# Performance work log

Measured on AMD Instinct MI355X. Metric: run time of the kernel, lower is better.

Reference implementation:

```python
import jax, jax.numpy as jnp
import numpy as np

N = 50000
D_IN = 128
D_OUT = 128
EPS = 1e-5


def setup_inputs() -> dict:
    key = jax.random.key(0)
    ks = jax.random.split(key, 10)
    x = jax.random.normal(ks[0], (N, D_IN), dtype=jnp.float32)
    edge_index = jax.random.randint(ks[1], (2, 800000), 0, N, dtype=jnp.int64)
    s_in = 1.0 / np.sqrt(D_IN)
    s_out = 1.0 / np.sqrt(D_OUT)
    return {
        "x": x,
        "edge_index": edge_index,
        # SAGEConv 1: lin_l (on aggregated neighbors, with bias), lin_r (root, no bias)
        "w1_l": jax.random.uniform(ks[2], (D_OUT, D_IN), jnp.float32, -s_in, s_in),
        "b1_l": jnp.zeros((D_OUT,), jnp.float32),
        "w1_r": jax.random.uniform(ks[3], (D_OUT, D_IN), jnp.float32, -s_in, s_in),
        # SAGEConv 2
        "w2_l": jax.random.uniform(ks[4], (D_OUT, D_OUT), jnp.float32, -s_out, s_out),
        "b2_l": jnp.zeros((D_OUT,), jnp.float32),
        "w2_r": jax.random.uniform(ks[5], (D_OUT, D_OUT), jnp.float32, -s_out, s_out),
        # BatchNorm affine params
        "bn_gamma": jnp.ones((D_OUT,), jnp.float32),
        "bn_beta": jnp.zeros((D_OUT,), jnp.float32),
    }


def _sage_conv(x, src, dst, w_l, b_l, w_r):
    # mean aggregation of source-node features into target nodes
    msg = x[src]                                              # [E, D]
    agg = jax.ops.segment_sum(msg, dst, num_segments=N)       # [N, D]
    cnt = jax.ops.segment_sum(jnp.ones((src.shape[0],), x.dtype), dst, num_segments=N)
    mean = agg / jnp.maximum(cnt, 1.0)[:, None]
    return mean @ w_l.T + b_l + x @ w_r.T


def _batch_norm(x, gamma, beta):
    mu = jnp.mean(x, axis=0)
    var = jnp.mean(jnp.square(x - mu), axis=0)  # biased, as in torch BN training
    return (x - mu) * jax.lax.rsqrt(var + EPS) * gamma + beta


def reference(x, edge_index, w1_l, b1_l, w1_r, w2_l, b2_l, w2_r, bn_gamma, bn_beta):
    src, dst = edge_index[0], edge_index[1]
    h = _sage_conv(x, src, dst, w1_l, b1_l, w1_r)
    h = _batch_norm(h, bn_gamma, bn_beta)
    h = jax.nn.relu(h)
    out = _sage_conv(h, src, dst, w2_l, b2_l, w2_r)
    return out
```

## Files before the change

kernel.cpp:

```cpp
#include <hip/hip_runtime.h>

#define D 128
#define EPS 1e-5f
#define FB_EPB 8

typedef unsigned int uint;
typedef __attribute__((ext_vector_type(4))) float f32x4;
typedef __attribute__((ext_vector_type(8))) short s16x8;

__device__ __forceinline__ uint pack_bf16(float a, float b)
{
    uint ua = __float_as_uint(a);
    uint ub = __float_as_uint(b);
    ua += 0x7FFFu + ((ua >> 16) & 1u);
    ub += 0x7FFFu + ((ub >> 16) & 1u);
    return (ua >> 16) | (ub & 0xFFFF0000u);
}
__device__ __forceinline__ float bf_lo(uint v) { return __uint_as_float(v << 16); }
__device__ __forceinline__ float bf_hi(uint v) { return __uint_as_float(v & 0xFFFF0000u); }

__global__ void prep_kernel(const float* __restrict__ x, uint* __restrict__ xb, int ncvt,
                            const float* __restrict__ w1l, const float* __restrict__ w1r,
                            const float* __restrict__ w2l, const float* __restrict__ w2r,
                            uint* __restrict__ wb1, uint* __restrict__ wb2)
{
    int idx = blockIdx.x * 256 + threadIdx.x;
    if (idx < ncvt) {
        float4 v = ((const float4*)x)[idx];
        uint2 o;
        o.x = pack_bf16(v.x, v.y);
        o.y = pack_bf16(v.z, v.w);
        ((uint2*)xb)[idx] = o;
    } else if (idx < ncvt + 8192) {
        int r = idx - ncvt;
        int layer = r >> 12;
        int rem = r & 4095;
        int lane = rem & 63;
        int knt = rem >> 6;
        int kstep = knt >> 3, nt = knt & 7;
        int nn = nt * 16 + (lane & 15);
        int kbase = kstep * 32 + (lane >> 4) * 8;
        const float* wl = layer ? w2l : w1l;
        const float* wr = layer ? w2r : w1r;
        uint* wb = layer ? wb2 : wb1;
        float v[8];
#pragma unroll
        for (int j = 0; j < 8; j++) {
            int k = kbase + j;
            v[j] = (k < D) ? wl[nn * D + k] : wr[nn * D + (k - D)];
        }
        uint4 o;
        o.x = pack_bf16(v[0], v[1]);
        o.y = pack_bf16(v[2], v[3]);
        o.z = pack_bf16(v[4], v[5]);
        o.w = pack_bf16(v[6], v[7]);
        ((uint4*)wb)[(kstep * 8 + nt) * 64 + lane] = o;
    }
}

__global__ __launch_bounds__(512) void bcount_kernel(const int* __restrict__ dst,
                                                     int* __restrict__ bcnt,
                                                     int E, int nblk, int nbuck)
{
    __shared__ int cnt[128];
    int t = threadIdx.x;
    if (t < 128) cnt[t] = 0;
    __syncthreads();
    int e0 = blockIdx.x * (512 * FB_EPB);
#pragma unroll
    for (int k = 0; k < FB_EPB; k++) {
        int e = e0 + k * 512 + t;
        if (e < E) atomicAdd(&cnt[dst[e] >> 9], 1);
    }
    __syncthreads();
    if (t < nbuck) bcnt[t * nblk + blockIdx.x] = cnt[t];
}

__global__ __launch_bounds__(1024) void bscan_kernel(int* __restrict__ bcnt, int M)
{
    __shared__ int sums[1024];
    int t = threadIdx.x;
    int chunk = (M + 1023) / 1024;
    int b0 = t * chunk;
    int b1 = min(b0 + chunk, M);
    int v[32];
    int s = 0;
    for (int i = b0; i < b1; i++) { v[i - b0] = bcnt[i]; s += v[i - b0]; }
    sums[t] = s;
    __syncthreads();
    for (int off = 1; off < 1024; off <<= 1) {
        int u = (t >= off) ? sums[t - off] : 0;
        __syncthreads();
        sums[t] += u;
        __syncthreads();
    }
    int run = sums[t] - s;
    for (int i = b0; i < b1; i++) { bcnt[i] = run; run += v[i - b0]; }
    if (t == 1023) bcnt[M] = sums[1023];
}

__global__ __launch_bounds__(512) void bscatter_kernel(const int* __restrict__ src,
                                                       const int* __restrict__ dst,
                                                       const int* __restrict__ bcnt,
                                                       uint2* __restrict__ ebuf,
                                                       int E, int nblk, int nbuck)
{
    __shared__ int cnt[128], base[128];
    int t = threadIdx.x;
    if (t < 128) cnt[t] = 0;
    __syncthreads();
    int e0 = blockIdx.x * (512 * FB_EPB);
    int s[FB_EPB], d[FB_EPB], loc[FB_EPB];
#pragma unroll
    for (int k = 0; k < FB_EPB; k++) {
        int e = e0 + k * 512 + t;
        if (e < E) {
            s[k] = src[e];
            d[k] = dst[e];
            loc[k] = atomicAdd(&cnt[d[k] >> 9], 1);
        }
    }
    __syncthreads();
    if (t < nbuck) base[t] = bcnt[t * nblk + blockIdx.x];
    __syncthreads();
#pragma unroll
    for (int k = 0; k < FB_EPB; k++) {
        int e = e0 + k * 512 + t;
        if (e < E) {
            int b = d[k] >> 9;
            ebuf[base[b] + loc[k]] = make_uint2((uint)s[k], (uint)d[k]);
        }
    }
}

__global__ __launch_bounds__(512) void pbuild_kernel(const int* __restrict__ bcnt,
                                                     const uint2* __restrict__ ebuf,
                                                     int* __restrict__ rowptr,
                                                     int* __restrict__ col,
                                                     int n, int nblk, int nbuck, int M, int E)
{
    __shared__ int lcnt[512], lscan[512];
    int t = threadIdx.x;
    int b = blockIdx.x;
    int nb = b << 9;
    int e0 = bcnt[b * nblk];
    int e1 = (b + 1 < nbuck) ? bcnt[(b + 1) * nblk] : bcnt[M];
    lcnt[t] = 0;
    __syncthreads();
    for (int i = e0 + t; i < e1; i += 512)
        atomicAdd(&lcnt[(int)ebuf[i].y - nb], 1);
    __syncthreads();
    int s = lcnt[t];
    lscan[t] = s;
    __syncthreads();
    for (int off = 1; off < 512; off <<= 1) {
        int u = (t >= off) ? lscan[t - off] : 0;
        __syncthreads();
        lscan[t] += u;
        __syncthreads();
    }
    int start = e0 + lscan[t] - s;
    int ncnt = min(512, n - nb);
    if (t < ncnt) rowptr[nb + t] = start;
    if (b == nbuck - 1 && t == 0) rowptr[n] = E;
    lscan[t] = start;
    __syncthreads();
    for (int i = e0 + t; i < e1; i += 512) {
        uint2 ed = ebuf[i];
        int p = atomicAdd(&lscan[(int)ed.y - nb], 1);
        col[p] = (int)ed.x;
    }
}

template<bool BN>
__global__ __launch_bounds__(256) void agg_kernel(const int* __restrict__ rowptr,
                                                  const int* __restrict__ col,
                                                  const uint* __restrict__ featb,
                                                  const float* __restrict__ scsh,
                                                  uint* __restrict__ aggb, int n)
{
    int node = blockIdx.x * 4 + (threadIdx.x >> 6);
    if (node >= n) return;
    int lane = threadIdx.x & 63;
    int sub = lane >> 4, l16 = lane & 15;
    int r0 = rowptr[node], r1 = rowptr[node + 1];
    uint4* out4 = (uint4*)aggb;
    if (r0 == r1) {
        if (lane < 16) out4[(size_t)node * 16 + l16] = make_uint4(0, 0, 0, 0);
        return;
    }
    float sc[8], sh[8];
    if (BN) {
        float4 s0 = ((const float4*)scsh)[l16 * 2];
        float4 s1 = ((const float4*)scsh)[l16 * 2 + 1];
        float4 t0 = ((const float4*)scsh)[32 + l16 * 2];
        float4 t1 = ((const float4*)scsh)[32 + l16 * 2 + 1];
        sc[0] = s0.x; sc[1] = s0.y; sc[2] = s0.z; sc[3] = s0.w;
        sc[4] = s1.x; sc[5] = s1.y; sc[6] = s1.z; sc[7] = s1.w;
        sh[0] = t0.x; sh[1] = t0.y; sh[2] = t0.z; sh[3] = t0.w;
        sh[4] = t1.x; sh[5] = t1.y; sh[6] = t1.z; sh[7] = t1.w;
    }
    float acc[8] = {0.f, 0.f, 0.f, 0.f, 0.f, 0.f, 0.f, 0.f};
    const uint4* fb = (const uint4*)featb;
    int last = r1 - 1;

    for (int i = r0; i < r1; i += 32) {
        uint4 v[8];
#pragma unroll
        for (int r = 0; r < 8; r++) {
            int idx = i + r * 4 + sub;
            int c = col[min(idx, last)];
            v[r] = fb[(size_t)c * 16 + l16];
        }
#pragma unroll
        for (int r = 0; r < 8; r++) {
            bool valid = (i + r * 4 + sub) < r1;
            uint4 u = v[r];
            float e[8] = {bf_lo(u.x), bf_hi(u.x), bf_lo(u.y), bf_hi(u.y),
                          bf_lo(u.z), bf_hi(u.z), bf_lo(u.w), bf_hi(u.w)};
#pragma unroll
            for (int j = 0; j < 8; j++) {
                float t = e[j];
                if (BN) t = fmaxf(t * sc[j] + sh[j], 0.f);
                acc[j] += valid ? t : 0.f;
            }
        }
    }
#pragma unroll
    for (int j = 0; j < 8; j++) {
        acc[j] += __shfl_down(acc[j], 32);
        acc[j] += __shfl_down(acc[j], 16);
    }
    if (lane < 16) {
        float inv = 1.0f / (float)(r1 - r0);
        uint4 o;
        o.x = pack_bf16(acc[0] * inv, acc[1] * inv);
        o.y = pack_bf16(acc[2] * inv, acc[3] * inv);
        o.z = pack_bf16(acc[4] * inv, acc[5] * inv);
        o.w = pack_bf16(acc[6] * inv, acc[7] * inv);
        out4[(size_t)node * 16 + l16] = o;
    }
}

#define TSTRIDE 132
template<bool FUSE1, bool BNP2>
__global__ __launch_bounds__(256) void conv_kernel(
    const uint* __restrict__ p1b, const uint* __restrict__ p2b,
    const uint* __restrict__ wb, const float* __restrict__ bias,
    const float* __restrict__ scsh, float* __restrict__ outf,
    uint* __restrict__ outb, float* __restrict__ pstats, int n)
{
    extern __shared__ float smem[];
    float* tile = smem;
    float* scs = smem;
    int w = threadIdx.x >> 6, lane = threadIdx.x & 63;
    int quad = lane >> 4, l15 = lane & 15;
    int nb = blockIdx.x * 64;

    if (BNP2) {
        scs[threadIdx.x] = scsh[threadIdx.x];
        __syncthreads();
    }

    const uint4* p1 = (const uint4*)p1b;
    const uint4* p2 = (const uint4*)p2b;
    const uint4* wv = (const uint4*)wb;

    uint4 B[8][2];
    int nt0 = w * 2;
#pragma unroll
    for (int ks = 0; ks < 8; ks++) {
#pragma unroll
        for (int t = 0; t < 2; t++)
            B[ks][t] = wv[(ks * 8 + nt0 + t) * 64 + lane];
    }

    float bv0 = bias[nt0 * 16 + l15];
    float bv1 = bias[nt0 * 16 + 16 + l15];

    for (int rt = 0; rt < 4; rt++) {
        int node = nb + rt * 16 + l15;
        int nc = min(node, n - 1);
        uint4 A[8];
#pragma unroll
        for (int ks = 0; ks < 4; ks++) A[ks] = p1[(size_t)nc * 16 + ks * 4 + quad];
#pragma unroll
        for (int ks = 0; ks < 4; ks++) A[ks + 4] = p2[(size_t)nc * 16 + ks * 4 + quad];

        if (BNP2) {
#pragma unroll
            for (int ks = 4; ks < 8; ks++) {
                int c0 = (ks - 4) * 32 + quad * 8;
                uint4 u = A[ks];
                float e[8] = {bf_lo(u.x), bf_hi(u.x), bf_lo(u.y), bf_hi(u.y),
                              bf_lo(u.z), bf_hi(u.z), bf_lo(u.w), bf_hi(u.w)};
#pragma unroll
                for (int j = 0; j < 8; j++)
                    e[j] = fmaxf(e[j] * scs[c0 + j] + scs[128 + c0 + j], 0.f);
                u.x = pack_bf16(e[0], e[1]);
                u.y = pack_bf16(e[2], e[3]);
                u.z = pack_bf16(e[4], e[5]);
                u.w = pack_bf16(e[6], e[7]);
                A[ks] = u;
            }
        }

        f32x4 acc0 = {bv0, bv0, bv0, bv0};
        f32x4 acc1 = {bv1, bv1, bv1, bv1};
#pragma unroll
        for (int ks = 0; ks < 8; ks++) {
            s16x8 a = *(s16x8*)&A[ks];
            acc0 = __builtin_amdgcn_mfma_f32_16x16x32_bf16(a, *(s16x8*)&B[ks][0], acc0, 0, 0, 0);
            acc1 = __builtin_amdgcn_mfma_f32_16x16x32_bf16(a, *(s16x8*)&B[ks][1], acc1, 0, 0, 0);
        }
        int row0 = nb + rt * 16 + quad * 4;
        int colbase = nt0 * 16 + l15;
        if (FUSE1) {
            int rloc0 = rt * 16 + quad * 4;
#pragma unroll
            for (int reg = 0; reg < 4; reg++) {
                bool ok = (row0 + reg) < n;
                tile[(rloc0 + reg) * TSTRIDE + colbase]      = ok ? acc0[reg] : 0.f;
                tile[(rloc0 + reg) * TSTRIDE + colbase + 16] = ok ? acc1[reg] : 0.f;
            }
        } else {
#pragma unroll
            for (int reg = 0; reg < 4; reg++) {
                int row = row0 + reg;
                if (row < n) {
                    outf[(size_t)row * D + colbase] = acc0[reg];
                    outf[(size_t)row * D + colbase + 16] = acc1[reg];
                }
            }
        }
    }

    if (FUSE1) {
        __syncthreads();
        int colj = threadIdx.x & 127, half = threadIdx.x >> 7;
        float s = 0.f, ss = 0.f;
        for (int r = half * 32; r < half * 32 + 32; r++) {
            float v = tile[r * TSTRIDE + colj];
            s += v;
            ss += v * v;
        }
        float* pb = pstats + (size_t)blockIdx.x * 512 + half * 256;
        pb[colj] = s;
        pb[128 + colj] = ss;
        uint4* ob4 = (uint4*)outb;
#pragma unroll
        for (int q4 = 0; q4 < 4; q4++) {
            int idx = q4 * 256 + threadIdx.x;
            int r = idx >> 4, q = idx & 15;
            int row = nb + r;
            if (row < n) {
                float* tr = &tile[r * TSTRIDE + q * 8];
                uint4 o;
                o.x = pack_bf16(tr[0], tr[1]);
                o.y = pack_bf16(tr[2], tr[3]);
                o.z = pack_bf16(tr[4], tr[5]);
                o.w = pack_bf16(tr[6], tr[7]);
                ob4[(size_t)row * 16 + q] = o;
            }
        }
    }
}

__global__ __launch_bounds__(256) void reduce_kernel(const float* __restrict__ pstats,
                                                     float* __restrict__ stats, int nparts)
{
    int j = threadIdx.x;
    int chunk = (nparts + gridDim.x - 1) / gridDim.x;
    int p0 = blockIdx.x * chunk;
    int p1 = min(p0 + chunk, nparts);
    float s = 0.f;
    for (int p = p0; p < p1; p++) s += pstats[(size_t)p * 256 + j];
    unsafeAtomicAdd(&stats[j], s);
}

__global__ void bnfin_kernel(const float* __restrict__ stats, const float* __restrict__ gamma,
                             const float* __restrict__ beta, float* __restrict__ scsh, float n_inv)
{
    int j = threadIdx.x;
    float mean = stats[j] * n_inv;
    float var = fmaxf(stats[128 + j] * n_inv - mean * mean, 0.f);
    float sc = gamma[j] * rsqrtf(var + EPS);
    scsh[j] = sc;
    scsh[128 + j] = beta[j] - mean * sc;
}

extern "C" void kernel_launch(void* const* d_in, const int* in_sizes, int n_in,
                              void* d_out, int out_size, void* d_ws, size_t ws_size,
                              hipStream_t stream)
{
    const float* x     = (const float*)d_in[0];
    const int*   ei    = (const int*)d_in[1];
    const float* w1_l  = (const float*)d_in[2];
    const float* b1_l  = (const float*)d_in[3];
    const float* w1_r  = (const float*)d_in[4];
    const float* w2_l  = (const float*)d_in[5];
    const float* b2_l  = (const float*)d_in[6];
    const float* w2_r  = (const float*)d_in[7];
    const float* gamma = (const float*)d_in[8];
    const float* beta  = (const float*)d_in[9];

    int N = in_sizes[0] / D;
    int E = in_sizes[1] / 2;
    const int* src = ei;
    const int* dst = ei + E;

    int cblocks = (N + 63) / 64;
    int nbuck   = (N + 511) >> 9;
    int nblk    = (E + 4095) / 4096;
    int M       = nbuck * nblk;

    uint*  aggb   = (uint*)d_ws;
    uint*  xb     = aggb + (size_t)N * 64;
    uint*  hb     = xb + (size_t)N * 64;
    uint*  wb1    = hb + (size_t)N * 64;
    uint*  wb2    = wb1 + 16384;
    uint2* ebuf   = (uint2*)(wb2 + 16384);
    float* stats  = (float*)(ebuf + E);
    float* scsh   = stats + 256;
    float* pstats = scsh + 256;
    int*   rowptr = (int*)(pstats + (size_t)cblocks * 512);
    int*   col    = rowptr + N + 1;
    int*   bcnt   = col + E;

    hipMemsetAsync(stats, 0, 256 * sizeof(float), stream);

    int ncvt = N * 32;
    int pblocks = (ncvt + 8192 + 255) / 256;
    prep_kernel<<<pblocks, 256, 0, stream>>>(x, xb, ncvt, w1_l, w1_r, w2_l, w2_r, wb1, wb2);

    int ablocks = (N + 3) / 4;

    bcount_kernel<<<nblk, 512, 0, stream>>>(dst, bcnt, E, nblk, nbuck);
    bscan_kernel<<<1, 1024, 0, stream>>>(bcnt, M);
    bscatter_kernel<<<nblk, 512, 0, stream>>>(src, dst, bcnt, ebuf, E, nblk, nbuck);
    pbuild_kernel<<<nbuck, 512, 0, stream>>>(bcnt, ebuf, rowptr, col, N, nblk, nbuck, M, E);

    agg_kernel<false><<<ablocks, 256, 0, stream>>>(rowptr, col, xb, nullptr, aggb, N);
    conv_kernel<true, false><<<cblocks, 256, 64 * TSTRIDE * 4, stream>>>(
        aggb, xb, wb1, b1_l, nullptr, nullptr, hb, pstats, N);

    reduce_kernel<<<32, 256, 0, stream>>>(pstats, stats, cblocks * 2);
    bnfin_kernel<<<1, 128, 0, stream>>>(stats, gamma, beta, scsh, 1.0f / (float)N);

    agg_kernel<true><<<ablocks, 256, 0, stream>>>(rowptr, col, hb, scsh, aggb, N);
    conv_kernel<false, true><<<cblocks, 256, 256 * 4, stream>>>(
        aggb, hb, wb2, b2_l, scsh, (float*)d_out, nullptr, nullptr, N);
}
```

Baseline: 265.2 us.

## Materialize BN+ReLU once in a separate pass and simplify gather loop with zero-row padding

Adds a bnapply kernel that writes normalized, ReLU'd bf16 features once, so the second aggregation and second conv no longer recompute BN+ReLU for every gathered edge. The gather loop drops from 8 to 4 rows per iteration. Invalid edges now point at an appended zero row instead of being masked with a select. The cost is an extra N×128 bf16 read/write pass, one more launch, and extra workspace for the padded buffers.

```diff
diff --git a/kernel.cpp b/kernel.cpp
--- a/kernel.cpp
+++ b/kernel.cpp
@@ -55,6 +55,8 @@
         o.z = pack_bf16(v[4], v[5]);
         o.w = pack_bf16(v[6], v[7]);
         ((uint4*)wb)[(kstep * 8 + nt) * 64 + lane] = o;
+    } else if (idx < ncvt + 8192 + 32) {
+        ((uint2*)xb)[ncvt + (idx - ncvt - 8192)] = make_uint2(0, 0);
     }
 }
 
@@ -172,11 +174,9 @@
     }
 }
 
-template<bool BN>
 __global__ __launch_bounds__(256) void agg_kernel(const int* __restrict__ rowptr,
                                                   const int* __restrict__ col,
                                                   const uint* __restrict__ featb,
-                                                  const float* __restrict__ scsh,
                                                   uint* __restrict__ aggb, int n)
 {
     int node = blockIdx.x * 4 + (threadIdx.x >> 6);
@@ -189,41 +189,26 @@
         if (lane < 16) out4[(size_t)node * 16 + l16] = make_uint4(0, 0, 0, 0);
         return;
     }
-    float sc[8], sh[8];
-    if (BN) {
-        float4 s0 = ((const float4*)scsh)[l16 * 2];
-        float4 s1 = ((const float4*)scsh)[l16 * 2 + 1];
-        float4 t0 = ((const float4*)scsh)[32 + l16 * 2];
-        float4 t1 = ((const float4*)scsh)[32 + l16 * 2 + 1];
-        sc[0] = s0.x; sc[1] = s0.y; sc[2] = s0.z; sc[3] = s0.w;
-        sc[4] = s1.x; sc[5] = s1.y; sc[6] = s1.z; sc[7] = s1.w;
-        sh[0] = t0.x; sh[1] = t0.y; sh[2] = t0.z; sh[3] = t0.w;
-        sh[4] = t1.x; sh[5] = t1.y; sh[6] = t1.z; sh[7] = t1.w;
-    }
     float acc[8] = {0.f, 0.f, 0.f, 0.f, 0.f, 0.f, 0.f, 0.f};
     const uint4* fb = (const uint4*)featb;
     int last = r1 - 1;
 
-    for (int i = r0; i < r1; i += 32) {
-        uint4 v[8];
-#pragma unroll
-        for (int r = 0; r < 8; r++) {
+    for (int i = r0; i < r1; i += 16) {
+        uint4 v[4];
+#pragma unroll
+        for (int r = 0; r < 4; r++) {
             int idx = i + r * 4 + sub;
-            int c = col[min(idx, last)];
+            int cl = col[min(idx, last)];
+            int c = (idx < r1) ? cl : n;
             v[r] = fb[(size_t)c * 16 + l16];
         }
 #pragma unroll
-        for (int r = 0; r < 8; r++) {
-            bool valid = (i + r * 4 + sub) < r1;
+        for (int r = 0; r < 4; r++) {
             uint4 u = v[r];
-            float e[8] = {bf_lo(u.x), bf_hi(u.x), bf_lo(u.y), bf_hi(u.y),
-                          bf_lo(u.z), bf_hi(u.z), bf_lo(u.w), bf_hi(u.w)};
-#pragma unroll
-            for (int j = 0; j < 8; j++) {
-                float t = e[j];
-                if (BN) t = fmaxf(t * sc[j] + sh[j], 0.f);
-                acc[j] += valid ? t : 0.f;
-            }
+            acc[0] += bf_lo(u.x); acc[1] += bf_hi(u.x);
+            acc[2] += bf_lo(u.y); acc[3] += bf_hi(u.y);
+            acc[4] += bf_lo(u.z); acc[5] += bf_hi(u.z);
+            acc[6] += bf_lo(u.w); acc[7] += bf_hi(u.w);
         }
     }
 #pragma unroll
@@ -243,24 +228,18 @@
 }
 
 #define TSTRIDE 132
-template<bool FUSE1, bool BNP2>
+template<bool FUSE1>
 __global__ __launch_bounds__(256) void conv_kernel(
     const uint* __restrict__ p1b, const uint* __restrict__ p2b,
     const uint* __restrict__ wb, const float* __restrict__ bias,
-    const float* __restrict__ scsh, float* __restrict__ outf,
-    uint* __restrict__ outb, float* __restrict__ pstats, int n)
+    float* __restrict__ outf, uint* __restrict__ outb,
+    float* __restrict__ pstats, int n)
 {
     extern __shared__ float smem[];
     float* tile = smem;
-    float* scs = smem;
     int w = threadIdx.x >> 6, lane = threadIdx.x & 63;
     int quad = lane >> 4, l15 = lane & 15;
     int nb = blockIdx.x * 64;
-
-    if (BNP2) {
-        scs[threadIdx.x] = scsh[threadIdx.x];
-        __syncthreads();
-    }
 
     const uint4* p1 = (const uint4*)p1b;
     const uint4* p2 = (const uint4*)p2b;
@@ -286,24 +265,6 @@
         for (int ks = 0; ks < 4; ks++) A[ks] = p1[(size_t)nc * 16 + ks * 4 + quad];
 #pragma unroll
         for (int ks = 0; ks < 4; ks++) A[ks + 4] = p2[(size_t)nc * 16 + ks * 4 + quad];
-
-        if (BNP2) {
-#pragma unroll
-            for (int ks = 4; ks < 8; ks++) {
-                int c0 = (ks - 4) * 32 + quad * 8;
-                uint4 u = A[ks];
-                float e[8] = {bf_lo(u.x), bf_hi(u.x), bf_lo(u.y), bf_hi(u.y),
-                              bf_lo(u.z), bf_hi(u.z), bf_lo(u.w), bf_hi(u.w)};
-#pragma unroll
-                for (int j = 0; j < 8; j++)
-                    e[j] = fmaxf(e[j] * scs[c0 + j] + scs[128 + c0 + j], 0.f);
-                u.x = pack_bf16(e[0], e[1]);
-                u.y = pack_bf16(e[2], e[3]);
-                u.z = pack_bf16(e[4], e[5]);
-                u.w = pack_bf16(e[6], e[7]);
-                A[ks] = u;
-            }
-        }
 
         f32x4 acc0 = {bv0, bv0, bv0, bv0};
         f32x4 acc1 = {bv1, bv1, bv1, bv1};
@@ -389,6 +350,29 @@
     scsh[128 + j] = beta[j] - mean * sc;
 }
 
+__global__ __launch_bounds__(256) void bnapply_kernel(const uint* __restrict__ hb,
+                                                      const float* __restrict__ scsh,
+                                                      uint* __restrict__ hbn, int total2)
+{
+    __shared__ float scs[256];
+    scs[threadIdx.x] = scsh[threadIdx.x];
+    __syncthreads();
+    int idx = blockIdx.x * 256 + threadIdx.x;
+    if (blockIdx.x == 0 && threadIdx.x < 32)
+        ((uint2*)hbn)[total2 + threadIdx.x] = make_uint2(0, 0);
+    if (idx >= total2) return;
+    int j4 = (idx & 31) * 4;
+    uint2 u = ((const uint2*)hb)[idx];
+    float e0 = fmaxf(bf_lo(u.x) * scs[j4 + 0] + scs[128 + j4 + 0], 0.f);
+    float e1 = fmaxf(bf_hi(u.x) * scs[j4 + 1] + scs[128 + j4 + 1], 0.f);
+    float e2 = fmaxf(bf_lo(u.y) * scs[j4 + 2] + scs[128 + j4 + 2], 0.f);
+    float e3 = fmaxf(bf_hi(u.y) * scs[j4 + 3] + scs[128 + j4 + 3], 0.f);
+    uint2 o;
+    o.x = pack_bf16(e0, e1);
+    o.y = pack_bf16(e2, e3);
+    ((uint2*)hbn)[idx] = o;
+}
+
 extern "C" void kernel_launch(void* const* d_in, const int* in_sizes, int n_in,
                               void* d_out, int out_size, void* d_ws, size_t ws_size,
                               hipStream_t stream)
@@ -416,8 +400,9 @@
 
     uint*  aggb   = (uint*)d_ws;
     uint*  xb     = aggb + (size_t)N * 64;
-    uint*  hb     = xb + (size_t)N * 64;
-    uint*  wb1    = hb + (size_t)N * 64;
+    uint*  hb     = xb + (size_t)(N + 1) * 64;
+    uint*  hbn    = hb + (size_t)N * 64;
+    uint*  wb1    = hbn + (size_t)(N + 1) * 64;
     uint*  wb2    = wb1 + 16384;
     uint2* ebuf   = (uint2*)(wb2 + 16384);
     float* stats  = (float*)(ebuf + E);
@@ -430,7 +415,7 @@
     hipMemsetAsync(stats, 0, 256 * sizeof(float), stream);
 
     int ncvt = N * 32;
-    int pblocks = (ncvt + 8192 + 255) / 256;
+    int pblocks = (ncvt + 8192 + 32 + 255) / 256;
     prep_kernel<<<pblocks, 256, 0, stream>>>(x, xb, ncvt, w1_l, w1_r, w2_l, w2_r, wb1, wb2);
 
     int ablocks = (N + 3) / 4;
@@ -440,14 +425,15 @@
     bscatter_kernel<<<nblk, 512, 0, stream>>>(src, dst, bcnt, ebuf, E, nblk, nbuck);
     pbuild_kernel<<<nbuck, 512, 0, stream>>>(bcnt, ebuf, rowptr, col, N, nblk, nbuck, M, E);
 
-    agg_kernel<false><<<ablocks, 256, 0, stream>>>(rowptr, col, xb, nullptr, aggb, N);
-    conv_kernel<true, false><<<cblocks, 256, 64 * TSTRIDE * 4, stream>>>(
-        aggb, xb, wb1, b1_l, nullptr, nullptr, hb, pstats, N);
+    agg_kernel<<<ablocks, 256, 0, stream>>>(rowptr, col, xb, aggb, N);
+    conv_kernel<true><<<cblocks, 256, 64 * TSTRIDE * 4, stream>>>(
+        aggb, xb, wb1, b1_l, nullptr, hb, pstats, N);
 
     reduce_kernel<<<32, 256, 0, stream>>>(pstats, stats, cblocks * 2);
     bnfin_kernel<<<1, 128, 0, stream>>>(stats, gamma, beta, scsh, 1.0f / (float)N);
-
-    agg_kernel<true><<<ablocks, 256, 0, stream>>>(rowptr, col, hb, scsh, aggb, N);
-    conv_kernel<false, true><<<cblocks, 256, 256 * 4, stream>>>(
-        aggb, hb, wb2, b2_l, scsh, (float*)d_out, nullptr, nullptr, N);
-}
+    bnapply_kernel<<<(N * 32 + 255) / 256, 256, 0, stream>>>(hb, scsh, hbn, N * 32);
+
+    agg_kernel<<<ablocks, 256, 0, stream>>>(rowptr, col, hbn, aggb, N);
+    conv_kernel<false><<<cblocks, 256, 1024, stream>>>(
+        aggb, hbn, wb2, b2_l, (float*)d_out, nullptr, nullptr, N);
+}
```

Result: faster. 252.5 us (-4.8%).
